# Performance work log

Measured on AMD Instinct MI355X. Metric: run time of the kernel, lower is better.

Reference implementation:

```python
import jax, jax.numpy as jnp
import numpy as np
import math

B, S, D_MODEL, HEADS, GRID = 4, 2048, 512, 8, 8
HEAD_DIM = D_MODEL // HEADS
A_C, K_C, C_C = 0.9724108095811765, 0.9884401790754128, 0.999449553483052


def setup_inputs() -> dict:
    key = jax.random.key(0)
    ks = jax.random.split(key, 4)
    q = jax.random.normal(ks[0], (B, S, D_MODEL), jnp.float32)
    mask = jnp.tril(jnp.ones((S, S), dtype=bool))[None, None]  # causal (1,1,S,S)
    out_dim = 3 * D_MODEL
    grid_norm = jnp.arange(1, GRID + 1, dtype=jnp.float32)  # (grid,)
    # is_first=True init: normal(0,0.4)/output_dim/grid_norm_factor
    amplitudes = jax.random.normal(ks[1], (out_dim, D_MODEL, GRID), jnp.float32) * 0.4 / out_dim / grid_norm
    # norm_freq with is_first=True -> freq = arange(1..grid) / (grid+1)**0 = arange
    freq = jnp.arange(1, GRID + 1, dtype=jnp.float32)  # (grid,)
    grid_phase = jnp.arange(1, GRID + 1, dtype=jnp.float32) / (GRID + 1)
    input_phase = jnp.linspace(0.0, math.pi, D_MODEL, dtype=jnp.float32)[:, None]  # (in,1)
    phase0 = grid_phase[None, :] + input_phase  # (in, grid)
    ratio = 1.0
    for i in range(1, GRID):
        ratio *= A_C * i ** (-K_C) + C_C
    phase = phase0 * np.float32(ratio)
    kan_bias = jnp.ones((out_dim,), jnp.float32) / out_dim
    lim = math.sqrt(6.0 / (D_MODEL + D_MODEL))  # xavier_uniform
    out_w = jax.random.uniform(ks[2], (D_MODEL, D_MODEL), jnp.float32, -lim, lim)
    out_b = jnp.zeros((D_MODEL,), jnp.float32)
    return {"q": q, "mask": mask, "freq": freq, "phase": phase,
            "amplitudes": amplitudes, "kan_bias": kan_bias,
            "out_w": out_w, "out_b": out_b}


def sinekan(x2d, freq, phase, amp, bias):
    # y[n,j] = sum_{k,l} sin(x[n,k]*f[l] + p[k,l]) * amp[j,k,l] + bias[j]
    # expand sin(a+p) = sin(a)cos(p) + cos(a)sin(p); fold phase into weights
    ang = x2d[:, :, None] * freq  # (N, in, grid)
    w_sin = amp * jnp.cos(phase)  # (out, in, grid)
    w_cos = amp * jnp.sin(phase)
    y = (jnp.einsum('nkl,jkl->nj', jnp.sin(ang), w_sin)
         + jnp.einsum('nkl,jkl->nj', jnp.cos(ang), w_cos))
    return y + bias


def rotate_half(u):
    u1, u2 = jnp.split(u, 2, axis=-1)
    return jnp.concatenate([-u2, u1], axis=-1)


def apply_rope(x, pos_emb):
    cos, sin = jnp.split(pos_emb, 2, axis=-1)  # each (S, head_dim//2)
    x_even, x_odd = x[..., ::2], x[..., 1::2]
    x1 = x_even * cos + rotate_half(x_odd) * sin
    x2 = x_odd * cos + rotate_half(x_even) * sin
    return jnp.concatenate([x1, x2], axis=-1)


def rope_emb(seq_len, dim):
    half = dim // 2
    inv_freq = 1.0 / (10000.0 ** (jnp.arange(half, dtype=jnp.float32) / half))
    ang = jnp.arange(seq_len, dtype=jnp.float32)[:, None] * inv_freq  # (S, half)
    return jnp.concatenate([jnp.cos(ang), jnp.sin(ang)], axis=-1)  # (S, dim)


def reference(q, mask, freq, phase, amplitudes, kan_bias, out_w, out_b):
    b, s, _ = q.shape
    qkv = sinekan(q.reshape(-1, D_MODEL), freq, phase, amplitudes, kan_bias)
    qkv = qkv.reshape(b, s, HEADS, 3 * HEAD_DIM).transpose(0, 2, 1, 3)  # (b,h,s,3d)
    qs, ks, vs = jnp.split(qkv, 3, axis=-1)
    pe = rope_emb(s, HEAD_DIM)
    qs = apply_rope(qs, pe)
    ks = apply_rope(ks, pe)
    scores = jnp.einsum('bhqd,bhkd->bhqk', qs, ks) / math.sqrt(HEAD_DIM)
    scores = jnp.where(mask, scores.astype(jnp.float32), -1e9)
    attn = jax.nn.softmax(scores, axis=-1)
    ctx = jnp.einsum('bhqk,bhkd->bhqd', attn, vs)
    ctx = ctx.transpose(0, 2, 1, 3).reshape(b, s, D_MODEL)
    return ctx @ out_w.T + out_b
```

## Files before the change

### kernel.cpp

```cpp
#include <hip/hip_runtime.h>
#include <math.h>


typedef __attribute__((ext_vector_type(8))) short bf16x8;
typedef __attribute__((ext_vector_type(8))) unsigned short ushort8;
typedef __attribute__((ext_vector_type(4))) unsigned short ushort4v;
typedef __attribute__((ext_vector_type(4))) float f32x4;

#define DEV __device__ __forceinline__

DEV unsigned short f2bf(float f) {
  unsigned u = __builtin_bit_cast(unsigned, f);
  u += 0x7FFFu + ((u >> 16) & 1u);
  return (unsigned short)(u >> 16);
}
DEV float bf2f(unsigned short h) {
  unsigned u = ((unsigned)h) << 16;
  return __builtin_bit_cast(float, u);
}

#define GLDS16(gp, lp)                                                         \
  __builtin_amdgcn_global_load_lds(                                            \
      (const __attribute__((address_space(1))) void*)(gp),                     \
      (__attribute__((address_space(3))) void*)(lp), 16, 0, 0)

__global__ __launch_bounds__(256) void wprep(const float* __restrict__ amp,
                                             const float* __restrict__ phase,
                                             unsigned short* __restrict__ Wb) {
  int id = blockIdx.x * 256 + threadIdx.x;
  int j = id >> 9;
  int k = id & 511;
  const float* ap = amp + (size_t)id * 8;
  const float* ph = phase + k * 8;
  union { unsigned short u[16]; uint4 v[2]; } pk;
#pragma unroll
  for (int l = 0; l < 8; ++l) {
    float sp, cp;
    sincosf(ph[l], &sp, &cp);
    float a = ap[l];
    pk.u[l] = f2bf(a * cp);
    pk.u[8 + l] = f2bf(a * sp);
  }
  uint4* dst = (uint4*)(Wb + (size_t)j * 8192 + k * 16);
  dst[0] = pk.v[0];
  dst[1] = pk.v[1];
}

__global__ __launch_bounds__(256) void owprep(const float* __restrict__ w,
                                              unsigned short* __restrict__ o) {
  int id = blockIdx.x * 256 + threadIdx.x;
  o[id] = f2bf(w[id]);
}

__global__ __launch_bounds__(256) void fgen(const float* __restrict__ q,
                                            unsigned short* __restrict__ F) {
  int id = blockIdx.x * 256 + threadIdx.x;
  int row = id >> 9;
  int dim = id & 511;
  float x = q[(size_t)row * 512 + dim];
  union { unsigned short u[16]; uint4 v[2]; } fr;
#pragma unroll
  for (int l = 1; l <= 8; ++l) {
    float a = x * (float)l;
    fr.u[l - 1] = f2bf(__sinf(a));
    fr.u[7 + l] = f2bf(__cosf(a));
  }
  uint4* dst = (uint4*)(F + (size_t)row * 8192 + dim * 16);
  dst[0] = fr.v[0];
  dst[1] = fr.v[1];
}

__global__ __launch_bounds__(512, 2) void kan_gemm8(
    const unsigned short* __restrict__ F, const unsigned short* __restrict__ Wb,
    const float* __restrict__ bias, unsigned short* __restrict__ qkv) {
  __shared__ __align__(16) char LDS[114688];

  const int tid = threadIdx.x, lane = tid & 63, wid = tid >> 6;
  const int wm = wid >> 2, wn = wid & 3;
  const int l15 = lane & 15, kg = lane >> 4;

  int bid = blockIdx.x;
  int xcd = bid & 7, u = bid >> 3;
  const int m0 = (xcd * 4 + (u & 3)) * 256;
  const int n0 = (u >> 2) * 192;

  const int growl = wid * 8 + (lane >> 3);
  const int cswz = ((lane & 7) ^ (lane >> 3)) << 4;

  f32x4 acc[2][4][3] = {};
  bf16x8 af[4][2], bf[3][2];

#define STAGE_A(T, C)                                                           \
  GLDS16((const char*)F + (size_t)(m0 + (C)*64 + growl) * 16384 +               \
             (size_t)(T) * 128 + cswz,                                          \
         LDS + (((T)&1) * 32768 + (C)*8192 + wid * 1024))

#define STAGE_B(T, C)                                                           \
  GLDS16((const char*)Wb + (size_t)(n0 + (C)*64 + growl) * 16384 +              \
             (size_t)(T) * 128 + cswz,                                          \
         LDS + (65536 + ((T)&1) * 24576 + (C)*8192 + wid * 1024))

#define DSREAD_A(T, MQ)                                                         \
  do {                                                                          \
    _Pragma("unroll") for (int mi = 0; mi < 4; ++mi)                            \
        _Pragma("unroll") for (int kk = 0; kk < 2; ++kk) {                      \
      int _r = (MQ)*128 + wm * 64 + mi * 16 + l15;                              \
      af[mi][kk] = *(const bf16x8*)(LDS + ((T)&1) * 32768 + _r * 128 +          \
                                    (((kk * 4 + kg) ^ (l15 & 7)) << 4));        \
    }                                                                           \
  } while (0)

#define DSREAD_B(T)                                                             \
  do {                                                                          \
    _Pragma("unroll") for (int ni = 0; ni < 3; ++ni)                            \
        _Pragma("unroll") for (int kk = 0; kk < 2; ++kk) {                      \
      int _r = wn * 48 + ni * 16 + l15;                                         \
      bf[ni][kk] = *(const bf16x8*)(LDS + 65536 + ((T)&1) * 24576 + _r * 128 +  \
                                    (((kk * 4 + kg) ^ (l15 & 7)) << 4));        \
    }                                                                           \
  } while (0)

#define MFMAS(MQ, NI0, NI1)                                                     \
  do {                                                                          \
    __builtin_amdgcn_s_setprio(1);                                              \
    _Pragma("unroll") for (int mi = 0; mi < 4; ++mi)                            \
        _Pragma("unroll") for (int ni = (NI0); ni <= (NI1); ++ni)               \
            _Pragma("unroll") for (int kk = 0; kk < 2; ++kk)                    \
                acc[MQ][mi][ni] = __builtin_amdgcn_mfma_f32_16x16x32_bf16(      \
                    af[mi][kk], bf[ni][kk], acc[MQ][mi][ni], 0, 0, 0);          \
    __builtin_amdgcn_s_setprio(0);                                              \
  } while (0)

#define BAR __builtin_amdgcn_s_barrier()
#define VMW(N) asm volatile("s_waitcnt vmcnt(" #N ")" ::: "memory")
#define LGW                                                                     \
  do {                                                                          \
    asm volatile("s_waitcnt lgkmcnt(0)" ::: "memory");                          \
    __builtin_amdgcn_sched_barrier(0);                                          \
  } while (0)

  STAGE_A(0, 0); STAGE_A(0, 1);
  STAGE_B(0, 0); STAGE_B(0, 1); STAGE_B(0, 2);
  STAGE_A(0, 2); STAGE_A(0, 3);

#pragma unroll 2
  for (int t = 0; t < 127; ++t) {
    VMW(2); BAR;
    DSREAD_A(t, 0); DSREAD_B(t);
    STAGE_A(t + 1, 0); STAGE_A(t + 1, 1);
    LGW; MFMAS(0, 0, 1);
    BAR;
    STAGE_B(t + 1, 0); STAGE_B(t + 1, 1);
    MFMAS(0, 2, 2);
    VMW(4); BAR;
    DSREAD_A(t, 1);
    STAGE_B(t + 1, 2); STAGE_A(t + 1, 2);
    LGW; MFMAS(1, 0, 1);
    BAR;
    STAGE_A(t + 1, 3);
    MFMAS(1, 2, 2);
  }
  {
    const int t = 127;
    VMW(2); BAR;
    DSREAD_A(t, 0); DSREAD_B(t);
    LGW; MFMAS(0, 0, 1);
    BAR;
    MFMAS(0, 2, 2);
    VMW(0); BAR;
    DSREAD_A(t, 1);
    LGW; MFMAS(1, 0, 1);
    BAR;
    MFMAS(1, 2, 2);
  }

#pragma unroll
  for (int mq = 0; mq < 2; ++mq)
#pragma unroll
    for (int mi = 0; mi < 4; ++mi)
#pragma unroll
      for (int ni = 0; ni < 3; ++ni) {
        int row = m0 + mq * 128 + wm * 64 + mi * 16 + kg * 4;
        int col = n0 + wn * 48 + ni * 16 + l15;
        float bv = bias[col];
        f32x4 a = acc[mq][mi][ni];
#pragma unroll
        for (int j = 0; j < 4; ++j)
          qkv[(size_t)(row + j) * 1536 + col] = f2bf(a[j] + bv);
      }
#undef STAGE_A
#undef STAGE_B
#undef DSREAD_A
#undef DSREAD_B
#undef MFMAS
#undef BAR
#undef VMW
#undef LGW
}

__global__ __launch_bounds__(256) void rope_prep(const unsigned short* __restrict__ qkv,
                                                 unsigned short* __restrict__ Qr,
                                                 unsigned short* __restrict__ Kr) {
  int id = blockIdx.x * 256 + threadIdx.x;
  int i = id & 31;
  int row = id >> 5;
  int s = row & 2047;
  int bh = row >> 11;
  int b = bh >> 3, h = bh & 7;

  const unsigned short* base = qkv + ((size_t)(b * 2048 + s)) * 1536 + h * 192;

  float inv = exp2f(-(float)i * (13.287712379549449f / 32.0f));
  float ang = (float)s * inv;
  float sn, cs;
  sincosf(ang, &sn, &cs);

  int pi = (i < 16) ? i + 16 : i - 16;
  float sign = (i < 16) ? -1.f : 1.f;
  size_t orow = (size_t)row * 64;

  {
    const unsigned short* xp = base;
    float xe = bf2f(xp[2 * i]), xo = bf2f(xp[2 * i + 1]);
    float po = bf2f(xp[2 * pi + 1]), pe = bf2f(xp[2 * pi]);
    Qr[orow + i] = f2bf(xe * cs + sign * po * sn);
    Qr[orow + 32 + i] = f2bf(xo * cs + sign * pe * sn);
  }
  {
    const unsigned short* xp = base + 64;
    float xe = bf2f(xp[2 * i]), xo = bf2f(xp[2 * i + 1]);
    float po = bf2f(xp[2 * pi + 1]), pe = bf2f(xp[2 * pi]);
    Kr[orow + i] = f2bf(xe * cs + sign * po * sn);
    Kr[orow + 32 + i] = f2bf(xo * cs + sign * pe * sn);
  }
}

__global__ __launch_bounds__(256) void attn(const unsigned short* __restrict__ Qr,
                                            const unsigned short* __restrict__ Kr,
                                            const unsigned short* __restrict__ qkv,
                                            unsigned short* __restrict__ ctx) {
  __shared__ __align__(16) unsigned short Klds[32 * 64];
  __shared__ __align__(16) unsigned short Vt[64 * 36];
  __shared__ __align__(16) unsigned short Plds[4 * 512];

  const int tid = threadIdx.x;
  const int lane = tid & 63;
  const int w = tid >> 6;
  const int qb = blockIdx.x;
  const int bh = blockIdx.y;
  const int b = bh >> 3, h = bh & 7;
  const int qw = qb * 64 + w * 16;
  const int l15 = lane & 15, kg = lane >> 4;

  const unsigned short* Qp = Qr + ((size_t)bh * 2048 + qw + l15) * 64 + kg * 8;
  bf16x8 qf0 = *(const bf16x8*)Qp;
  bf16x8 qf1 = *(const bf16x8*)(Qp + 32);

  f32x4 octx[4] = {};
  float den[4] = {0.f, 0.f, 0.f, 0.f};
  unsigned short* Pw = &Plds[w * 512];

  const int skp = tid >> 3;
  const int sds = tid & 7;
  const int vd = tid & 63;
  const int vkq = tid >> 6;

  const int nkt = 2 * qb + 2;
  for (int kt = 0; kt < nkt; ++kt) {
    ushort8 kv =
        *(const ushort8*)(Kr + ((size_t)bh * 2048 + kt * 32 + skp) * 64 + sds * 8);
    *(ushort8*)((char*)Klds + ((skp * 128 + sds * 16) ^ ((skp & 7) << 4))) = kv;
    {
      const unsigned short* vcol = qkv +
          ((size_t)(b * 2048 + kt * 32 + vkq * 8)) * 1536 + h * 192 + 128 + vd;
      ushort4v lo, hi;
      lo.x = vcol[0];
      lo.y = vcol[1536];
      lo.z = vcol[2 * 1536];
      lo.w = vcol[3 * 1536];
      hi.x = vcol[4 * 1536];
      hi.y = vcol[5 * 1536];
      hi.z = vcol[6 * 1536];
      hi.w = vcol[7 * 1536];
      *(ushort4v*)&Vt[vd * 36 + vkq * 8] = lo;
      *(ushort4v*)&Vt[vd * 36 + vkq * 8 + 4] = hi;
    }
    __syncthreads();

    f32x4 zero = {0.f, 0.f, 0.f, 0.f};
#pragma unroll
    for (int f = 0; f < 2; ++f) {
      int kp = f * 16 + l15;
      int swk = (kp & 7) << 4;
      bf16x8 kf0 = *(const bf16x8*)((char*)Klds + ((kp * 128 + kg * 16) ^ swk));
      bf16x8 kf1 = *(const bf16x8*)((char*)Klds + ((kp * 128 + 64 + kg * 16) ^ swk));
      f32x4 sA = __builtin_amdgcn_mfma_f32_16x16x32_bf16(qf0, kf0, zero, 0, 0, 0);
      sA = __builtin_amdgcn_mfma_f32_16x16x32_bf16(qf1, kf1, sA, 0, 0, 0);
      int kgl = kt * 32 + kp;
#pragma unroll
      for (int j = 0; j < 4; ++j) {
        int qrow = qw + kg * 4 + j;
        float p = (kgl <= qrow) ? __expf(sA[j] * 0.125f) : 0.f;
        den[j] += p;
        int prow = kg * 4 + j;
        *(unsigned short*)((char*)Pw +
                           ((prow * 64 + kp * 2) ^ ((prow & 3) << 4))) = f2bf(p);
      }
    }
    bf16x8 pf =
        *(const bf16x8*)((char*)Pw + ((l15 * 64 + kg * 16) ^ ((l15 & 3) << 4)));
#pragma unroll
    for (int nd = 0; nd < 4; ++nd) {
      int d = nd * 16 + l15;
      union { ushort4v h[2]; bf16x8 v; } vfu;
      vfu.h[0] = *(const ushort4v*)&Vt[d * 36 + kg * 8];
      vfu.h[1] = *(const ushort4v*)&Vt[d * 36 + kg * 8 + 4];
      octx[nd] = __builtin_amdgcn_mfma_f32_16x16x32_bf16(pf, vfu.v, octx[nd], 0, 0, 0);
    }
    __syncthreads();
  }

#pragma unroll
  for (int j = 0; j < 4; ++j) {
    float d_ = den[j];
    d_ += __shfl_xor(d_, 1);
    d_ += __shfl_xor(d_, 2);
    d_ += __shfl_xor(d_, 4);
    d_ += __shfl_xor(d_, 8);
    den[j] = d_;
  }
#pragma unroll
  for (int nd = 0; nd < 4; ++nd)
#pragma unroll
    for (int j = 0; j < 4; ++j) {
      int qrow = qw + kg * 4 + j;
      int col = h * 64 + nd * 16 + l15;
      ctx[((size_t)b * 2048 + qrow) * 512 + col] = f2bf(octx[nd][j] / den[j]);
    }
}

__global__ __launch_bounds__(256) void out_gemm(const unsigned short* __restrict__ A,
                                                const unsigned short* __restrict__ Bw,
                                                const float* __restrict__ outb,
                                                float* __restrict__ out) {
  __shared__ __align__(16) unsigned short Al[128 * 32];
  __shared__ __align__(16) unsigned short Bl[128 * 32];
  const int tid = threadIdx.x, lane = tid & 63, w = tid >> 6;
  const int wm = w >> 1, wn = w & 1;
  const int m0 = blockIdx.x * 128, n0 = blockIdx.y * 128;
  const int l15 = lane & 15, kg = lane >> 4;

  f32x4 acc[4][4] = {};

  const unsigned short* ga = A + (size_t)(m0 + (tid >> 2)) * 512 + (tid & 3) * 8;
  const unsigned short* gb = Bw + (size_t)(n0 + (tid >> 2)) * 512 + (tid & 3) * 8;

  for (int t = 0; t < 16; ++t) {
    GLDS16(ga + t * 32, &Al[w * 512]);
    GLDS16(ga + t * 32 + 64 * 512, &Al[2048 + w * 512]);
    GLDS16(gb + t * 32, &Bl[w * 512]);
    GLDS16(gb + t * 32 + 64 * 512, &Bl[2048 + w * 512]);
    __syncthreads();

    bf16x8 af[4], bfr[4];
#pragma unroll
    for (int m = 0; m < 4; ++m)
      af[m] = *(const bf16x8*)&Al[(wm * 64 + m * 16 + l15) * 32 + kg * 8];
#pragma unroll
    for (int n = 0; n < 4; ++n)
      bfr[n] = *(const bf16x8*)&Bl[(wn * 64 + n * 16 + l15) * 32 + kg * 8];
#pragma unroll
    for (int m = 0; m < 4; ++m)
#pragma unroll
      for (int n = 0; n < 4; ++n)
        acc[m][n] =
            __builtin_amdgcn_mfma_f32_16x16x32_bf16(af[m], bfr[n], acc[m][n], 0, 0, 0);

    __syncthreads();
  }

  const int rb = m0 + wm * 64 + kg * 4;
  const int cb = n0 + wn * 64 + l15;
#pragma unroll
  for (int n = 0; n < 4; ++n) {
    int cc = cb + n * 16;
    float bv = outb[cc];
#pragma unroll
    for (int m = 0; m < 4; ++m)
#pragma unroll
      for (int j = 0; j < 4; ++j)
        out[(size_t)(rb + m * 16 + j) * 512 + cc] = acc[m][n][j] + bv;
  }
}

extern "C" void kernel_launch(void* const* d_in, const int* in_sizes, int n_in,
                              void* d_out, int out_size, void* d_ws, size_t ws_size,
                              hipStream_t stream) {
  const float* q = (const float*)d_in[0];
  const float* phase = (const float*)d_in[3];
  const float* amp = (const float*)d_in[4];
  const float* kbias = (const float*)d_in[5];
  const float* out_w = (const float*)d_in[6];
  const float* out_b = (const float*)d_in[7];
  float* out = (float*)d_out;

  char* p = (char*)d_ws;
  unsigned short* Wb = (unsigned short*)(p);
  unsigned short* qkv = (unsigned short*)(p + 25165824);
  unsigned short* Qr = (unsigned short*)(p + 50331648);
  unsigned short* Kr = (unsigned short*)(p + 58720256);
  unsigned short* ctx = (unsigned short*)(p + 67108864);
  unsigned short* Wob = (unsigned short*)(p + 75497472);
  unsigned short* F = (unsigned short*)(p + 76021760);

  owprep<<<1024, 256, 0, stream>>>(out_w, Wob);
  wprep<<<3072, 256, 0, stream>>>(amp, phase, Wb);
  fgen<<<16384, 256, 0, stream>>>(q, F);
  kan_gemm8<<<256, 512, 0, stream>>>(F, Wb, kbias, qkv);
  rope_prep<<<8192, 256, 0, stream>>>(qkv, Qr, Kr);
  attn<<<dim3(32, 32), 256, 0, stream>>>(Qr, Kr, qkv, ctx);
  out_gemm<<<dim3(64, 4), 256, 0, stream>>>(ctx, Wob, out_b, out);
}
```

Measured before the change: 319.9 us.

## Retile KAN GEMM to 128x384 blocks and double attention key tile to 64

The SineKAN GEMM block tile changes from 256x192 to 128x384, with a new staging and LDS layout (128 KB), a three-phase k-step pipeline over B sub-panels and each wave covering 64x96 outputs. The attention kernel processes 64 keys per iteration instead of 32. It also stores V transposed with an XOR swizzle using 16-byte writes, and pads the P buffer rows. These changes are meant to raise operand reuse and cut barrier and loop overhead per key. In exchange they use more LDS and registers, which may lower occupancy.

```diff
diff --git a/kernel.cpp b/kernel.cpp
--- a/kernel.cpp
+++ b/kernel.cpp
@@ -4,7 +4,6 @@
 
 typedef __attribute__((ext_vector_type(8))) short bf16x8;
 typedef __attribute__((ext_vector_type(8))) unsigned short ushort8;
-typedef __attribute__((ext_vector_type(4))) unsigned short ushort4v;
 typedef __attribute__((ext_vector_type(4))) float f32x4;
 
 #define DEV __device__ __forceinline__
@@ -73,7 +72,7 @@
 __global__ __launch_bounds__(512, 2) void kan_gemm8(
     const unsigned short* __restrict__ F, const unsigned short* __restrict__ Wb,
     const float* __restrict__ bias, unsigned short* __restrict__ qkv) {
-  __shared__ __align__(16) char LDS[114688];
+  __shared__ __align__(16) char LDS[131072];
 
   const int tid = threadIdx.x, lane = tid & 63, wid = tid >> 6;
   const int wm = wid >> 2, wn = wid & 3;
@@ -81,53 +80,57 @@
 
   int bid = blockIdx.x;
   int xcd = bid & 7, u = bid >> 3;
-  const int m0 = (xcd * 4 + (u & 3)) * 256;
-  const int n0 = (u >> 2) * 192;
-
-  const int growl = wid * 8 + (lane >> 3);
-  const int cswz = ((lane & 7) ^ (lane >> 3)) << 4;
-
-  f32x4 acc[2][4][3] = {};
-  bf16x8 af[4][2], bf[3][2];
-
-#define STAGE_A(T, C)                                                           \
-  GLDS16((const char*)F + (size_t)(m0 + (C)*64 + growl) * 16384 +               \
+  const int m0 = (xcd * 8 + (u >> 2)) * 128;
+  const int n0 = (u & 3) * 384;
+
+  const int lrow = lane >> 3;
+  const int cswz = ((lane & 7) ^ lrow) << 4;
+
+  const int sg1 = wid >> 2, ss = wid & 3;
+  const int sg2 = sg1 + 2;
+
+  f32x4 acc[4][6] = {};
+  bf16x8 af[4][2], bf[2][2];
+
+#define STAGE_A(T, DB, C)                                                       \
+  GLDS16((const char*)F + (size_t)(m0 + (C)*64 + wid * 8 + lrow) * 16384 +      \
              (size_t)(T) * 128 + cswz,                                          \
-         LDS + (((T)&1) * 32768 + (C)*8192 + wid * 1024))
-
-#define STAGE_B(T, C)                                                           \
-  GLDS16((const char*)Wb + (size_t)(n0 + (C)*64 + growl) * 16384 +              \
+         LDS + ((DB)*16384 + ((C)*64 + wid * 8) * 128))
+
+#define STAGE_B(T, DB, G, P)                                                    \
+  GLDS16((const char*)Wb +                                                      \
+             (size_t)(n0 + (G)*96 + (P)*32 + ss * 8 + lrow) * 16384 +           \
              (size_t)(T) * 128 + cswz,                                          \
-         LDS + (65536 + ((T)&1) * 24576 + (C)*8192 + wid * 1024))
-
-#define DSREAD_A(T, MQ)                                                         \
+         LDS + (32768 + (DB)*49152 + ((G)*96 + (P)*32 + ss * 8) * 128))
+
+#define DSREAD_A(BUF)                                                           \
   do {                                                                          \
     _Pragma("unroll") for (int mi = 0; mi < 4; ++mi)                            \
         _Pragma("unroll") for (int kk = 0; kk < 2; ++kk) {                      \
-      int _r = (MQ)*128 + wm * 64 + mi * 16 + l15;                              \
-      af[mi][kk] = *(const bf16x8*)(LDS + ((T)&1) * 32768 + _r * 128 +          \
+      int _r = wm * 64 + mi * 16 + l15;                                         \
+      af[mi][kk] = *(const bf16x8*)(LDS + (BUF)*16384 + _r * 128 +              \
                                     (((kk * 4 + kg) ^ (l15 & 7)) << 4));        \
     }                                                                           \
   } while (0)
 
-#define DSREAD_B(T)                                                             \
+#define DSREAD_B(BUF, P)                                                        \
   do {                                                                          \
-    _Pragma("unroll") for (int ni = 0; ni < 3; ++ni)                            \
+    _Pragma("unroll") for (int q = 0; q < 2; ++q)                               \
         _Pragma("unroll") for (int kk = 0; kk < 2; ++kk) {                      \
-      int _r = wn * 48 + ni * 16 + l15;                                         \
-      bf[ni][kk] = *(const bf16x8*)(LDS + 65536 + ((T)&1) * 24576 + _r * 128 +  \
-                                    (((kk * 4 + kg) ^ (l15 & 7)) << 4));        \
+      int _r = wn * 96 + (P)*32 + q * 16 + l15;                                 \
+      bf[q][kk] = *(const bf16x8*)(LDS + 32768 + (BUF)*49152 + _r * 128 +       \
+                                   (((kk * 4 + kg) ^ (l15 & 7)) << 4));         \
     }                                                                           \
   } while (0)
 
-#define MFMAS(MQ, NI0, NI1)                                                     \
+#define MFMAS(P)                                                                \
   do {                                                                          \
     __builtin_amdgcn_s_setprio(1);                                              \
     _Pragma("unroll") for (int mi = 0; mi < 4; ++mi)                            \
-        _Pragma("unroll") for (int ni = (NI0); ni <= (NI1); ++ni)               \
+        _Pragma("unroll") for (int q = 0; q < 2; ++q)                           \
             _Pragma("unroll") for (int kk = 0; kk < 2; ++kk)                    \
-                acc[MQ][mi][ni] = __builtin_amdgcn_mfma_f32_16x16x32_bf16(      \
-                    af[mi][kk], bf[ni][kk], acc[MQ][mi][ni], 0, 0, 0);          \
+                acc[mi][(P)*2 + q] = __builtin_amdgcn_mfma_f32_16x16x32_bf16(   \
+                    af[mi][kk], bf[q][kk], acc[mi][(P)*2 + q], 0, 0, 0);        \
     __builtin_amdgcn_s_setprio(0);                                              \
   } while (0)
 
@@ -139,60 +142,66 @@
     __builtin_amdgcn_sched_barrier(0);                                          \
   } while (0)
 
-  STAGE_A(0, 0); STAGE_A(0, 1);
-  STAGE_B(0, 0); STAGE_B(0, 1); STAGE_B(0, 2);
-  STAGE_A(0, 2); STAGE_A(0, 3);
-
-#pragma unroll 2
-  for (int t = 0; t < 127; ++t) {
+#define KSTEP(T, BUF)                                                           \
+  do {                                                                          \
+                             \
+    VMW(4); BAR;                                                                \
+    DSREAD_A(BUF); DSREAD_B(BUF, 0);                                            \
+    STAGE_A((T) + 1, 1 - (BUF), 0); STAGE_A((T) + 1, 1 - (BUF), 1);             \
+    STAGE_B((T) + 1, 1 - (BUF), sg1, 0); STAGE_B((T) + 1, 1 - (BUF), sg2, 0);   \
+    LGW; MFMAS(0);                                                              \
+                                              \
+    VMW(6); BAR;                                                                \
+    DSREAD_B(BUF, 1);                                                           \
+    STAGE_B((T) + 1, 1 - (BUF), sg1, 1); STAGE_B((T) + 1, 1 - (BUF), sg2, 1);   \
+    LGW; MFMAS(1);                                                              \
+                                              \
+    VMW(6); BAR;                                                                \
+    DSREAD_B(BUF, 2);                                                           \
+    STAGE_B((T) + 1, 1 - (BUF), sg1, 2); STAGE_B((T) + 1, 1 - (BUF), sg2, 2);   \
+    LGW; MFMAS(2);                                                              \
+  } while (0)
+
+  STAGE_A(0, 0, 0); STAGE_A(0, 0, 1);
+  STAGE_B(0, 0, sg1, 0); STAGE_B(0, 0, sg2, 0);
+  STAGE_B(0, 0, sg1, 1); STAGE_B(0, 0, sg2, 1);
+  STAGE_B(0, 0, sg1, 2); STAGE_B(0, 0, sg2, 2);
+
+  for (int t = 0; t < 126; t += 2) {
+    KSTEP(t, 0);
+    KSTEP(t + 1, 1);
+  }
+  KSTEP(126, 0);
+  {
+    VMW(4); BAR;
+    DSREAD_A(1); DSREAD_B(1, 0);
+    LGW; MFMAS(0);
     VMW(2); BAR;
-    DSREAD_A(t, 0); DSREAD_B(t);
-    STAGE_A(t + 1, 0); STAGE_A(t + 1, 1);
-    LGW; MFMAS(0, 0, 1);
-    BAR;
-    STAGE_B(t + 1, 0); STAGE_B(t + 1, 1);
-    MFMAS(0, 2, 2);
-    VMW(4); BAR;
-    DSREAD_A(t, 1);
-    STAGE_B(t + 1, 2); STAGE_A(t + 1, 2);
-    LGW; MFMAS(1, 0, 1);
-    BAR;
-    STAGE_A(t + 1, 3);
-    MFMAS(1, 2, 2);
-  }
-  {
-    const int t = 127;
-    VMW(2); BAR;
-    DSREAD_A(t, 0); DSREAD_B(t);
-    LGW; MFMAS(0, 0, 1);
-    BAR;
-    MFMAS(0, 2, 2);
+    DSREAD_B(1, 1);
+    LGW; MFMAS(1);
     VMW(0); BAR;
-    DSREAD_A(t, 1);
-    LGW; MFMAS(1, 0, 1);
-    BAR;
-    MFMAS(1, 2, 2);
-  }
-
-#pragma unroll
-  for (int mq = 0; mq < 2; ++mq)
-#pragma unroll
-    for (int mi = 0; mi < 4; ++mi)
-#pragma unroll
-      for (int ni = 0; ni < 3; ++ni) {
-        int row = m0 + mq * 128 + wm * 64 + mi * 16 + kg * 4;
-        int col = n0 + wn * 48 + ni * 16 + l15;
-        float bv = bias[col];
-        f32x4 a = acc[mq][mi][ni];
-#pragma unroll
-        for (int j = 0; j < 4; ++j)
-          qkv[(size_t)(row + j) * 1536 + col] = f2bf(a[j] + bv);
-      }
+    DSREAD_B(1, 2);
+    LGW; MFMAS(2);
+  }
+
+#pragma unroll
+  for (int mi = 0; mi < 4; ++mi)
+#pragma unroll
+    for (int ni = 0; ni < 6; ++ni) {
+      int row = m0 + wm * 64 + mi * 16 + kg * 4;
+      int col = n0 + wn * 96 + ni * 16 + l15;
+      float bv = bias[col];
+      f32x4 a = acc[mi][ni];
+#pragma unroll
+      for (int j = 0; j < 4; ++j)
+        qkv[(size_t)(row + j) * 1536 + col] = f2bf(a[j] + bv);
+    }
 #undef STAGE_A
 #undef STAGE_B
 #undef DSREAD_A
 #undef DSREAD_B
 #undef MFMAS
+#undef KSTEP
 #undef BAR
 #undef VMW
 #undef LGW
@@ -239,9 +248,9 @@
                                             const unsigned short* __restrict__ Kr,
                                             const unsigned short* __restrict__ qkv,
                                             unsigned short* __restrict__ ctx) {
-  __shared__ __align__(16) unsigned short Klds[32 * 64];
-  __shared__ __align__(16) unsigned short Vt[64 * 36];
-  __shared__ __align__(16) unsigned short Plds[4 * 512];
+  __shared__ __align__(16) char KB[8192];
+  __shared__ __align__(16) char VT[8192];
+  __shared__ __align__(16) char PL[9216];
 
   const int tid = threadIdx.x;
   const int lane = tid & 63;
@@ -258,64 +267,61 @@
 
   f32x4 octx[4] = {};
   float den[4] = {0.f, 0.f, 0.f, 0.f};
-  unsigned short* Pw = &Plds[w * 512];
+  char* Pw = PL + w * 2304;
 
   const int skp = tid >> 3;
   const int sds = tid & 7;
   const int vd = tid & 63;
   const int vkq = tid >> 6;
 
-  const int nkt = 2 * qb + 2;
+  const int nkt = qb + 1;
   for (int kt = 0; kt < nkt; ++kt) {
-    ushort8 kv =
-        *(const ushort8*)(Kr + ((size_t)bh * 2048 + kt * 32 + skp) * 64 + sds * 8);
-    *(ushort8*)((char*)Klds + ((skp * 128 + sds * 16) ^ ((skp & 7) << 4))) = kv;
-    {
-      const unsigned short* vcol = qkv +
-          ((size_t)(b * 2048 + kt * 32 + vkq * 8)) * 1536 + h * 192 + 128 + vd;
-      ushort4v lo, hi;
-      lo.x = vcol[0];
-      lo.y = vcol[1536];
-      lo.z = vcol[2 * 1536];
-      lo.w = vcol[3 * 1536];
-      hi.x = vcol[4 * 1536];
-      hi.y = vcol[5 * 1536];
-      hi.z = vcol[6 * 1536];
-      hi.w = vcol[7 * 1536];
-      *(ushort4v*)&Vt[vd * 36 + vkq * 8] = lo;
-      *(ushort4v*)&Vt[vd * 36 + vkq * 8 + 4] = hi;
+#pragma unroll
+    for (int r = 0; r < 2; ++r) {
+      int krow = r * 32 + skp;
+      ushort8 kv = *(const ushort8*)(Kr + ((size_t)bh * 2048 + kt * 64 + krow) * 64 +
+                                     sds * 8);
+      *(ushort8*)(KB + ((krow * 128 + sds * 16) ^ ((krow & 7) << 4))) = kv;
+      const unsigned short* vcol =
+          qkv + ((size_t)(b * 2048 + kt * 64 + r * 32 + vkq * 8)) * 1536 +
+          h * 192 + 128 + vd;
+      ushort8 vv;
+#pragma unroll
+      for (int jj = 0; jj < 8; ++jj) vv[jj] = vcol[jj * 1536];
+      int slot = r * 4 + vkq;
+      *(ushort8*)(VT + (vd * 128 + ((slot * 16) ^ ((vd & 7) << 4)))) = vv;
     }
     __syncthreads();
 
     f32x4 zero = {0.f, 0.f, 0.f, 0.f};
 #pragma unroll
-    for (int f = 0; f < 2; ++f) {
+    for (int f = 0; f < 4; ++f) {
       int kp = f * 16 + l15;
       int swk = (kp & 7) << 4;
-      bf16x8 kf0 = *(const bf16x8*)((char*)Klds + ((kp * 128 + kg * 16) ^ swk));
-      bf16x8 kf1 = *(const bf16x8*)((char*)Klds + ((kp * 128 + 64 + kg * 16) ^ swk));
+      bf16x8 kf0 = *(const bf16x8*)(KB + ((kp * 128 + kg * 16) ^ swk));
+      bf16x8 kf1 = *(const bf16x8*)(KB + ((kp * 128 + 64 + kg * 16) ^ swk));
       f32x4 sA = __builtin_amdgcn_mfma_f32_16x16x32_bf16(qf0, kf0, zero, 0, 0, 0);
       sA = __builtin_amdgcn_mfma_f32_16x16x32_bf16(qf1, kf1, sA, 0, 0, 0);
-      int kgl = kt * 32 + kp;
+      int kgl = kt * 64 + kp;
 #pragma unroll
       for (int j = 0; j < 4; ++j) {
         int qrow = qw + kg * 4 + j;
         float p = (kgl <= qrow) ? __expf(sA[j] * 0.125f) : 0.f;
         den[j] += p;
         int prow = kg * 4 + j;
-        *(unsigned short*)((char*)Pw +
-                           ((prow * 64 + kp * 2) ^ ((prow & 3) << 4))) = f2bf(p);
+        *(unsigned short*)(Pw + prow * 144 + kp * 2) = f2bf(p);
       }
     }
-    bf16x8 pf =
-        *(const bf16x8*)((char*)Pw + ((l15 * 64 + kg * 16) ^ ((l15 & 3) << 4)));
+    bf16x8 pf0 = *(const bf16x8*)(Pw + l15 * 144 + kg * 16);
+    bf16x8 pf1 = *(const bf16x8*)(Pw + l15 * 144 + 64 + kg * 16);
 #pragma unroll
     for (int nd = 0; nd < 4; ++nd) {
       int d = nd * 16 + l15;
-      union { ushort4v h[2]; bf16x8 v; } vfu;
-      vfu.h[0] = *(const ushort4v*)&Vt[d * 36 + kg * 8];
-      vfu.h[1] = *(const ushort4v*)&Vt[d * 36 + kg * 8 + 4];
-      octx[nd] = __builtin_amdgcn_mfma_f32_16x16x32_bf16(pf, vfu.v, octx[nd], 0, 0, 0);
+      int swv = (d & 7) << 4;
+      bf16x8 vf0 = *(const bf16x8*)(VT + (d * 128 + ((kg * 16) ^ swv)));
+      bf16x8 vf1 = *(const bf16x8*)(VT + (d * 128 + ((64 + kg * 16) ^ swv)));
+      octx[nd] = __builtin_amdgcn_mfma_f32_16x16x32_bf16(pf0, vf0, octx[nd], 0, 0, 0);
+      octx[nd] = __builtin_amdgcn_mfma_f32_16x16x32_bf16(pf1, vf1, octx[nd], 0, 0, 0);
     }
     __syncthreads();
   }
```

Result: faster. 310.0 us (-3.1%).

## Double-buffer attention K/V via async LDS loads with pre-transposed V

Applied to the files above, without the earlier changes.

Adds a separate kernel that writes V transposed and XOR-swizzled into the scratch buffer, and pre-swizzles K in rope_prep. The attention kernel now uses 512 threads and 128 query rows per block, with 64-key tiles. K/V tiles are double-buffered through global_load_lds so the next tile loads while the current one computes, and the causal mask is skipped on fully visible tiles. fgen also replaces eight sin/cos evaluations with one sincos plus angle-addition recurrences. The trade-offs are an extra kernel pass over V and some accumulated error in the recurrence.

```diff
diff --git a/kernel.cpp b/kernel.cpp
--- a/kernel.cpp
+++ b/kernel.cpp
@@ -4,7 +4,6 @@
 
 typedef __attribute__((ext_vector_type(8))) short bf16x8;
 typedef __attribute__((ext_vector_type(8))) unsigned short ushort8;
-typedef __attribute__((ext_vector_type(4))) unsigned short ushort4v;
 typedef __attribute__((ext_vector_type(4))) float f32x4;
 
 #define DEV __device__ __forceinline__
@@ -58,12 +57,19 @@
   int row = id >> 9;
   int dim = id & 511;
   float x = q[(size_t)row * 512 + dim];
+  float s1, c1;
+  sincosf(x, &s1, &c1);
   union { unsigned short u[16]; uint4 v[2]; } fr;
-#pragma unroll
-  for (int l = 1; l <= 8; ++l) {
-    float a = x * (float)l;
-    fr.u[l - 1] = f2bf(__sinf(a));
-    fr.u[7 + l] = f2bf(__cosf(a));
+  float s = s1, c = c1;
+  fr.u[0] = f2bf(s);
+  fr.u[8] = f2bf(c);
+#pragma unroll
+  for (int l = 1; l < 8; ++l) {
+    float ns = s * c1 + c * s1;
+    float nc = c * c1 - s * s1;
+    s = ns; c = nc;
+    fr.u[l] = f2bf(s);
+    fr.u[8 + l] = f2bf(c);
   }
   uint4* dst = (uint4*)(F + (size_t)row * 8192 + dim * 16);
   dst[0] = fr.v[0];
@@ -230,18 +236,50 @@
     const unsigned short* xp = base + 64;
     float xe = bf2f(xp[2 * i]), xo = bf2f(xp[2 * i + 1]);
     float po = bf2f(xp[2 * pi + 1]), pe = bf2f(xp[2 * pi]);
-    Kr[orow + i] = f2bf(xe * cs + sign * po * sn);
-    Kr[orow + 32 + i] = f2bf(xo * cs + sign * pe * sn);
-  }
-}
-
-__global__ __launch_bounds__(256) void attn(const unsigned short* __restrict__ Qr,
+    int sw = s & 7;
+    int p1 = (((i >> 3) ^ sw) << 3) | (i & 7);
+    int p2 = (((4 + (i >> 3)) ^ sw) << 3) | (i & 7);
+    Kr[orow + p1] = f2bf(xe * cs + sign * po * sn);
+    Kr[orow + p2] = f2bf(xo * cs + sign * pe * sn);
+  }
+}
+
+__global__ __launch_bounds__(256) void vtr(const unsigned short* __restrict__ qkv,
+                                           unsigned short* __restrict__ Vt) {
+  __shared__ unsigned short T[64][72];
+  const int st = blockIdx.x, bh = blockIdx.y;
+  const int b = bh >> 3, h = bh & 7;
+  const int tid = threadIdx.x;
+  const int sl = tid >> 3, ds = tid & 7;
+#pragma unroll
+  for (int r = 0; r < 2; ++r) {
+    int s = st * 64 + r * 32 + sl;
+    ushort8 v = *(const ushort8*)(qkv + ((size_t)(b * 2048 + s)) * 1536 +
+                                  h * 192 + 128 + ds * 8);
+#pragma unroll
+    for (int j = 0; j < 8; ++j) T[r * 32 + sl][ds * 8 + j] = v[j];
+  }
+  __syncthreads();
+  const int d = tid & 63, sq = tid >> 6;
+  ushort8 lo, hi;
+#pragma unroll
+  for (int j = 0; j < 8; ++j) {
+    lo[j] = T[sq * 16 + j][d];
+    hi[j] = T[sq * 16 + 8 + j][d];
+  }
+  size_t basee = ((size_t)(bh * 64 + d)) * 2048 + st * 64;
+  int sw = d & 7;
+  *(ushort8*)(Vt + basee + (((sq * 2) ^ sw) << 3)) = lo;
+  *(ushort8*)(Vt + basee + (((sq * 2 + 1) ^ sw) << 3)) = hi;
+}
+
+__global__ __launch_bounds__(512) void attn(const unsigned short* __restrict__ Qr,
                                             const unsigned short* __restrict__ Kr,
-                                            const unsigned short* __restrict__ qkv,
+                                            const unsigned short* __restrict__ Vt,
                                             unsigned short* __restrict__ ctx) {
-  __shared__ __align__(16) unsigned short Klds[32 * 64];
-  __shared__ __align__(16) unsigned short Vt[64 * 36];
-  __shared__ __align__(16) unsigned short Plds[4 * 512];
+  __shared__ __align__(16) char KB[2][8192];
+  __shared__ __align__(16) char VT[2][8192];
+  __shared__ __align__(16) char PL[18432];
 
   const int tid = threadIdx.x;
   const int lane = tid & 63;
@@ -249,7 +287,7 @@
   const int qb = blockIdx.x;
   const int bh = blockIdx.y;
   const int b = bh >> 3, h = bh & 7;
-  const int qw = qb * 64 + w * 16;
+  const int qw = qb * 128 + w * 16;
   const int l15 = lane & 15, kg = lane >> 4;
 
   const unsigned short* Qp = Qr + ((size_t)bh * 2048 + qw + l15) * 64 + kg * 8;
@@ -258,66 +296,64 @@
 
   f32x4 octx[4] = {};
   float den[4] = {0.f, 0.f, 0.f, 0.f};
-  unsigned short* Pw = &Plds[w * 512];
-
-  const int skp = tid >> 3;
-  const int sds = tid & 7;
-  const int vd = tid & 63;
-  const int vkq = tid >> 6;
+  char* Pw = PL + w * 2304;
+
+  const int srow = tid >> 3, sslot = tid & 7;
+  const unsigned short* Ksrc = Kr + (size_t)bh * 2048 * 64;
+  const unsigned short* Vsrc = Vt + ((size_t)(bh * 64 + srow)) * 2048;
+
+#define STAGEKV(KT, BUF)                                                        \
+  do {                                                                          \
+    GLDS16((const char*)(Ksrc + ((size_t)((KT)*64 + srow) * 64 + sslot * 8)),   \
+           KB[BUF] + tid * 16);                                                 \
+    GLDS16((const char*)(Vsrc + ((size_t)(KT)*64 + sslot * 8)),                 \
+           VT[BUF] + tid * 16);                                                 \
+  } while (0)
 
   const int nkt = 2 * qb + 2;
+  STAGEKV(0, 0);
   for (int kt = 0; kt < nkt; ++kt) {
-    ushort8 kv =
-        *(const ushort8*)(Kr + ((size_t)bh * 2048 + kt * 32 + skp) * 64 + sds * 8);
-    *(ushort8*)((char*)Klds + ((skp * 128 + sds * 16) ^ ((skp & 7) << 4))) = kv;
-    {
-      const unsigned short* vcol = qkv +
-          ((size_t)(b * 2048 + kt * 32 + vkq * 8)) * 1536 + h * 192 + 128 + vd;
-      ushort4v lo, hi;
-      lo.x = vcol[0];
-      lo.y = vcol[1536];
-      lo.z = vcol[2 * 1536];
-      lo.w = vcol[3 * 1536];
-      hi.x = vcol[4 * 1536];
-      hi.y = vcol[5 * 1536];
-      hi.z = vcol[6 * 1536];
-      hi.w = vcol[7 * 1536];
-      *(ushort4v*)&Vt[vd * 36 + vkq * 8] = lo;
-      *(ushort4v*)&Vt[vd * 36 + vkq * 8 + 4] = hi;
-    }
-    __syncthreads();
-
+    const int buf = kt & 1;
+    asm volatile("s_waitcnt vmcnt(0)" ::: "memory");
+    __builtin_amdgcn_s_barrier();
+    if (kt + 1 < nkt) STAGEKV(kt + 1, buf ^ 1);
+
+    const bool full = (kt * 64 + 63 <= qw);
     f32x4 zero = {0.f, 0.f, 0.f, 0.f};
-#pragma unroll
-    for (int f = 0; f < 2; ++f) {
+    __builtin_amdgcn_s_setprio(1);
+#pragma unroll
+    for (int f = 0; f < 4; ++f) {
       int kp = f * 16 + l15;
       int swk = (kp & 7) << 4;
-      bf16x8 kf0 = *(const bf16x8*)((char*)Klds + ((kp * 128 + kg * 16) ^ swk));
-      bf16x8 kf1 = *(const bf16x8*)((char*)Klds + ((kp * 128 + 64 + kg * 16) ^ swk));
+      bf16x8 kf0 = *(const bf16x8*)(KB[buf] + ((kp * 128 + kg * 16) ^ swk));
+      bf16x8 kf1 = *(const bf16x8*)(KB[buf] + ((kp * 128 + 64 + kg * 16) ^ swk));
       f32x4 sA = __builtin_amdgcn_mfma_f32_16x16x32_bf16(qf0, kf0, zero, 0, 0, 0);
       sA = __builtin_amdgcn_mfma_f32_16x16x32_bf16(qf1, kf1, sA, 0, 0, 0);
-      int kgl = kt * 32 + kp;
+      int kgl = kt * 64 + kp;
 #pragma unroll
       for (int j = 0; j < 4; ++j) {
-        int qrow = qw + kg * 4 + j;
-        float p = (kgl <= qrow) ? __expf(sA[j] * 0.125f) : 0.f;
+        float p = __expf(sA[j] * 0.125f);
+        if (!full) {
+          int qrow = qw + kg * 4 + j;
+          p = (kgl <= qrow) ? p : 0.f;
+        }
         den[j] += p;
         int prow = kg * 4 + j;
-        *(unsigned short*)((char*)Pw +
-                           ((prow * 64 + kp * 2) ^ ((prow & 3) << 4))) = f2bf(p);
+        *(unsigned short*)(Pw + prow * 144 + kp * 2) = f2bf(p);
       }
     }
-    bf16x8 pf =
-        *(const bf16x8*)((char*)Pw + ((l15 * 64 + kg * 16) ^ ((l15 & 3) << 4)));
+    bf16x8 pf0 = *(const bf16x8*)(Pw + l15 * 144 + kg * 16);
+    bf16x8 pf1 = *(const bf16x8*)(Pw + l15 * 144 + 64 + kg * 16);
 #pragma unroll
     for (int nd = 0; nd < 4; ++nd) {
       int d = nd * 16 + l15;
-      union { ushort4v h[2]; bf16x8 v; } vfu;
-      vfu.h[0] = *(const ushort4v*)&Vt[d * 36 + kg * 8];
-      vfu.h[1] = *(const ushort4v*)&Vt[d * 36 + kg * 8 + 4];
-      octx[nd] = __builtin_amdgcn_mfma_f32_16x16x32_bf16(pf, vfu.v, octx[nd], 0, 0, 0);
+      int swv = (d & 7) << 4;
+      bf16x8 vf0 = *(const bf16x8*)(VT[buf] + (d * 128 + ((kg * 16) ^ swv)));
+      bf16x8 vf1 = *(const bf16x8*)(VT[buf] + (d * 128 + ((64 + kg * 16) ^ swv)));
+      octx[nd] = __builtin_amdgcn_mfma_f32_16x16x32_bf16(pf0, vf0, octx[nd], 0, 0, 0);
+      octx[nd] = __builtin_amdgcn_mfma_f32_16x16x32_bf16(pf1, vf1, octx[nd], 0, 0, 0);
     }
-    __syncthreads();
+    __builtin_amdgcn_s_setprio(0);
   }
 
 #pragma unroll
@@ -412,12 +448,14 @@
   unsigned short* ctx = (unsigned short*)(p + 67108864);
   unsigned short* Wob = (unsigned short*)(p + 75497472);
   unsigned short* F = (unsigned short*)(p + 76021760);
+  unsigned short* Vt = (unsigned short*)(p);
 
   owprep<<<1024, 256, 0, stream>>>(out_w, Wob);
   wprep<<<3072, 256, 0, stream>>>(amp, phase, Wb);
   fgen<<<16384, 256, 0, stream>>>(q, F);
   kan_gemm8<<<256, 512, 0, stream>>>(F, Wb, kbias, qkv);
   rope_prep<<<8192, 256, 0, stream>>>(qkv, Qr, Kr);
-  attn<<<dim3(32, 32), 256, 0, stream>>>(Qr, Kr, qkv, ctx);
+  vtr<<<dim3(32, 32), 256, 0, stream>>>(qkv, Vt);
+  attn<<<dim3(16, 32), 512, 0, stream>>>(Qr, Kr, Vt, ctx);
   out_gemm<<<dim3(64, 4), 256, 0, stream>>>(ctx, Wob, out_b, out);
 }
```

Measured after the change: 309.5 us. -3.3%, faster.
